# Kernel optimization log

Measured on AMD Instinct MI355X. Metric: run time of the kernel, lower is better.

Reference implementation:

```python
import jax, jax.numpy as jnp
import numpy as np

N = 50000
E = 800000
IN_DIM = 256
HID = 128
HALF = HID // 2
OUT_DIM = 2


def setup_inputs() -> dict:
    key = jax.random.key(0)
    ks = jax.random.split(key, 16)
    s = lambda fan_in: 1.0 / np.sqrt(fan_in)
    inp = {
        "x": jax.random.normal(ks[0], (N, IN_DIM), dtype=jnp.float32),
        "edge_index": jax.random.randint(ks[1], (2, E), 0, N, dtype=jnp.int64),
        # lin_in: input_dim -> hidden
        "W_in": jax.random.uniform(ks[2], (IN_DIM, HID), jnp.float32, -s(IN_DIM), s(IN_DIM)),
        "b_in": jnp.zeros((HID,), jnp.float32),
        # lin_nor / lin_abnor: half -> hidden
        "W_nor": jax.random.uniform(ks[3], (HALF, HID), jnp.float32, -s(HALF), s(HALF)),
        "b_nor": jnp.zeros((HID,), jnp.float32),
        "W_abnor": jax.random.uniform(ks[4], (HALF, HID), jnp.float32, -s(HALF), s(HALF)),
        "b_abnor": jnp.zeros((HID,), jnp.float32),
        # attention gate
        "W_att": jax.random.uniform(ks[5], (HID, HID), jnp.float32, -s(HID), s(HID)),
        "b_att": jnp.zeros((HID,), jnp.float32),
        "v_att": jax.random.uniform(ks[6], (HID, 1), jnp.float32, -s(HID), s(HID)),
        # update linear
        "W_upd": jax.random.uniform(ks[7], (HID, HID), jnp.float32, -s(HID), s(HID)),
        "b_upd": jnp.zeros((HID,), jnp.float32),
        # classifier
        "W_cls": jax.random.uniform(ks[8], (HID, OUT_DIM), jnp.float32, -s(HID), s(HID)),
        "b_cls": jnp.zeros((OUT_DIM,), jnp.float32),
    }
    return inp


def reference(x, edge_index, W_in, b_in, W_nor, b_nor, W_abnor, b_abnor,
              W_att, b_att, v_att, W_upd, b_upd, W_cls, b_cls):
    n = x.shape[0]
    # add self loops (add_self_loops)
    loops = jnp.tile(jnp.arange(n, dtype=edge_index.dtype), (2, 1))
    ei = jnp.concatenate([edge_index, loops], axis=1)
    row, col = ei[0], ei[1]  # row = source j, col = target i

    # lin_in + leaky_relu (dropout p=0 / eval)
    h = jax.nn.leaky_relu(x @ W_in + b_in)

    # split halves and project
    x_nor = h[:, :HALF] @ W_nor + b_nor      # [N, HID]
    x_abnor = h[:, HALF:] @ W_abnor + b_abnor

    # symmetric normalization by target degree
    deg = jax.ops.segment_sum(jnp.ones_like(col, dtype=h.dtype), col, num_segments=n)
    dinv = jnp.where(deg > 0, jax.lax.rsqrt(jnp.where(deg > 0, deg, 1.0)), 0.0)
    norm = dinv[row] * dinv[col]             # [E']

    # per-edge gather
    xn_j = x_nor[row]                        # [E', HID]
    xa_j = x_abnor[row]

    # denoising attention gate: sigmoid(v^T tanh(W(xn+xa)+b))
    h_att = jnp.tanh((xn_j + xa_j) @ W_att + b_att)
    alpha = jax.nn.sigmoid(h_att @ v_att)    # [E', 1]

    msg = norm[:, None] * (alpha * xn_j + (1.0 - alpha) * xa_j)

    # scatter-add to targets
    aggr = jax.ops.segment_sum(msg, col, num_segments=n)  # [N, HID]

    upd = aggr @ W_upd + b_upd
    out = jax.nn.leaky_relu(upd) @ W_cls + b_cls
    return out
```

## Files before the change

kernel.cpp:

```cpp
#include <hip/hip_runtime.h>

#define N_NODES 50000
#define E_EDGES 800000
#define IN_DIM  256
#define HID     128
#define HALF    64
#define OUT_DIM 2
#define NW      32
#define SLOPE   0.01f

#define ST      132
#define WSLICE  (NW * ST)

#define SSTRIDE 520
#define PLANE   (8 * SSTRIDE)

#define SCAN_B  512
#define SCAN_NB ((N_NODES + SCAN_B - 1) / SCAN_B)

typedef unsigned int uint32;
typedef __attribute__((ext_vector_type(8)))  __bf16 bf16x8v;
typedef __attribute__((ext_vector_type(16))) float  f32x16;

union BF8 { bf16x8v v; unsigned short s[8]; uint4 q; };

#define FI_F 0
#define FN_F 4096
#define FA_F 5120
#define FT_F 6144
#define FU_F 8192
#define F_TOTAL 10240

__device__ __forceinline__ uint32 rne16u(uint32 u) {
    return (u + 0x7fffu + ((u >> 16) & 1u)) >> 16;
}

__device__ __forceinline__ uint32 pack_hl(float v) {
    uint32 uu = __float_as_uint(v);
    uint32 hh = rne16u(uu);
    float  fh = __uint_as_float(hh << 16);
    float  r  = v - fh;
    uint32 ll = rne16u(__float_as_uint(r));
    return (hh << 16) | ll;
}

__device__ __forceinline__ float fast_tanh(float x) {
    float ex = __expf(2.f * x);
    return 1.f - 2.f * __builtin_amdgcn_rcpf(ex + 1.f);
}
__device__ __forceinline__ float fast_sig(float x) {
    return __builtin_amdgcn_rcpf(1.f + __expf(-x));
}

__device__ __forceinline__ void mfma3(f32x16& acc, bf16x8v ah, bf16x8v al,
                                      bf16x8v bh, bf16x8v bl) {
    acc = __builtin_amdgcn_mfma_f32_32x32x16_bf16(ah, bh, acc, 0, 0, 0);
    acc = __builtin_amdgcn_mfma_f32_32x32x16_bf16(ah, bl, acc, 0, 0, 0);
    acc = __builtin_amdgcn_mfma_f32_32x32x16_bf16(al, bh, acc, 0, 0, 0);
}

__device__ __forceinline__ void stage_split4(__bf16* __restrict__ Ahi,
                                             __bf16* __restrict__ Alo,
                                             int rr, int k, float4 v) {
    int s_idx = k >> 4, jb = k & 7, lt = rr + 32 * ((k >> 3) & 1);
    int base = s_idx * SSTRIDE + lt * 8 + jb;
    float f[4] = {v.x, v.y, v.z, v.w};
    uint32 h[4], lo[4];
    #pragma unroll
    for (int j = 0; j < 4; j++) {
        uint32 uu = __float_as_uint(f[j]);
        uint32 hh = rne16u(uu);
        float  fh = __uint_as_float(hh << 16);
        float  r  = f[j] - fh;
        h[j] = hh; lo[j] = rne16u(__float_as_uint(r));
    }
    *(uint2*)(Ahi + base) = make_uint2(h[0] | (h[1] << 16), h[2] | (h[3] << 16));
    *(uint2*)(Alo + base) = make_uint2(lo[0] | (lo[1] << 16), lo[2] | (lo[3] << 16));
}

__device__ __forceinline__ void mfma_gemm1_pre(f32x16& acc,
        const __bf16* __restrict__ Ahi, const __bf16* __restrict__ Alo,
        int S, int sg0, const uint4* __restrict__ F, int fbase, int l, int t) {
    for (int s = 0; s < S; s++) {
        bf16x8v ah = *(const bf16x8v*)&Ahi[s * SSTRIDE + l * 8];
        bf16x8v al = *(const bf16x8v*)&Alo[s * SSTRIDE + l * 8];
        int f = fbase + ((sg0 + s) * 4 + t) * 64 + l;
        BF8 bh, bl; bh.q = F[2 * f]; bl.q = F[2 * f + 1];
        mfma3(acc, ah, al, bh.v, bl.v);
    }
}

__device__ __forceinline__ void mfma_gemm1_pk(f32x16& acc, const uint32* T,
        int aoff, int S, const uint4* __restrict__ F, int fbase, int l, int t) {
    const int row = l & 31, khi = 8 * (l >> 5);
    for (int s = 0; s < S; s++) {
        int k0 = aoff + 16 * s + khi;
        uint4 qa = *(const uint4*)&T[row * ST + k0];
        uint4 qb = *(const uint4*)&T[row * ST + k0 + 4];
        BF8 ah, al;
        ah.q.x = (qa.x >> 16) | (qa.y & 0xffff0000u);
        ah.q.y = (qa.z >> 16) | (qa.w & 0xffff0000u);
        ah.q.z = (qb.x >> 16) | (qb.y & 0xffff0000u);
        ah.q.w = (qb.z >> 16) | (qb.w & 0xffff0000u);
        al.q.x = (qa.x & 0xffffu) | (qa.y << 16);
        al.q.y = (qa.z & 0xffffu) | (qa.w << 16);
        al.q.z = (qb.x & 0xffffu) | (qb.y << 16);
        al.q.w = (qb.z & 0xffffu) | (qb.w << 16);
        int f = fbase + (s * 4 + t) * 64 + l;
        BF8 bh, bl; bh.q = F[2 * f]; bl.q = F[2 * f + 1];
        mfma3(acc, ah.v, al.v, bh.v, bl.v);
    }
}

__device__ __forceinline__ uint32 pack_bf2(float x, float y) {
    return rne16u(__float_as_uint(x)) | (rne16u(__float_as_uint(y)) << 16);
}

__global__ void zero_int_kernel(int* __restrict__ p, int n) {
    int i = blockIdx.x * blockDim.x + threadIdx.x;
    if (i < n) p[i] = 0;
}

__global__ void deg_ticket_kernel(const int* __restrict__ col,
                                  int* __restrict__ cnt, int* __restrict__ ticket) {
    int e = blockIdx.x * blockDim.x + threadIdx.x;
    if (e < E_EDGES) ticket[e] = atomicAdd(&cnt[col[e]], 1);
}

__device__ __forceinline__ int wave_iscan(int v, int l) {
    #pragma unroll
    for (int off = 1; off < 64; off <<= 1) {
        int t = __shfl_up(v, off, 64);
        if (l >= off) v += t;
    }
    return v;
}

__global__ __launch_bounds__(SCAN_B) void scan1_kernel(
    const int* __restrict__ cnt, int* __restrict__ row_start, int* __restrict__ bsum)
{
    __shared__ int wsum[SCAN_B / 64];
    int i = blockIdx.x * SCAN_B + threadIdx.x;
    int v = (i < N_NODES) ? cnt[i] : 0;
    int l = threadIdx.x & 63, w = threadIdx.x >> 6;
    int isc = wave_iscan(v, l);
    if (l == 63) wsum[w] = isc;
    __syncthreads();
    int wo = 0;
    #pragma unroll
    for (int k = 0; k < SCAN_B / 64; k++) wo += (k < w) ? wsum[k] : 0;
    if (i < N_NODES) row_start[i] = wo + isc - v;
    if (threadIdx.x == SCAN_B - 1) bsum[blockIdx.x] = wo + isc;
}

__global__ __launch_bounds__(128) void scan2_kernel(
    int* __restrict__ bsum, int* __restrict__ row_start)
{
    __shared__ int wsum[2];
    int i = threadIdx.x;
    int v = (i < SCAN_NB) ? bsum[i] : 0;
    int l = i & 63, w = i >> 6;
    int isc = wave_iscan(v, l);
    if (l == 63) wsum[w] = isc;
    __syncthreads();
    int wo = (w == 1) ? wsum[0] : 0;
    if (i < SCAN_NB) bsum[i] = wo + isc - v;
    if (i == SCAN_NB - 1) row_start[N_NODES] = wo + isc;
}

__global__ __launch_bounds__(SCAN_B) void scan3_kernel(
    const int* __restrict__ bsum, int* __restrict__ row_start)
{
    int i = blockIdx.x * SCAN_B + threadIdx.x;
    if (i < N_NODES) row_start[i] += bsum[blockIdx.x];
}

__global__ void fill_kernel(const int* __restrict__ ei,
                            const int* __restrict__ row_start,
                            const int* __restrict__ ticket,
                            int* __restrict__ csr_src)
{
    int e = blockIdx.x * blockDim.x + threadIdx.x;
    if (e >= E_EDGES) return;
    int j = ei[e];
    int i = ei[E_EDGES + e];
    csr_src[row_start[i] + ticket[e]] = j;
}

__global__ __launch_bounds__(256) void prep_w_kernel(
    const float* __restrict__ W_in, const float* __restrict__ W_nor,
    const float* __restrict__ W_ab, const float* __restrict__ W_att,
    const float* __restrict__ W_upd,
    uint4* __restrict__ F)
{
    int idx = blockIdx.x * 256 + threadIdx.x;
    const float* W; int fbase, fi;
    if (idx < 4096)       { W = W_in;  fbase = FI_F; fi = idx; }
    else if (idx < 5120)  { W = W_nor; fbase = FN_F; fi = idx - 4096; }
    else if (idx < 6144)  { W = W_ab;  fbase = FA_F; fi = idx - 5120; }
    else if (idx < 8192)  { W = W_att; fbase = FT_F; fi = idx - 6144; }
    else if (idx < 10240) { W = W_upd; fbase = FU_F; fi = idx - 8192; }
    else return;
    int l = fi & 63, st = fi >> 6, t = st & 3, s = st >> 2;
    int k0 = 16 * s + 8 * (l >> 5);
    int c  = 32 * t + (l & 31);
    uint32 hi[8], lo[8];
    #pragma unroll
    for (int j = 0; j < 8; j++) {
        float v = W[(size_t)(k0 + j) * HID + c];
        uint32 uu = __float_as_uint(v);
        uint32 h  = rne16u(uu);
        float  fh = __uint_as_float(h << 16);
        float  r  = v - fh;
        hi[j] = h;
        lo[j] = rne16u(__float_as_uint(r));
    }
    uint4 H, L;
    H.x = hi[0] | (hi[1] << 16); H.y = hi[2] | (hi[3] << 16);
    H.z = hi[4] | (hi[5] << 16); H.w = hi[6] | (hi[7] << 16);
    L.x = lo[0] | (lo[1] << 16); L.y = lo[2] | (lo[3] << 16);
    L.z = lo[4] | (lo[5] << 16); L.w = lo[6] | (lo[7] << 16);
    int f = fbase + fi;
    F[2 * f]     = H;
    F[2 * f + 1] = L;
}

__global__ __launch_bounds__(256, 4) void node_phase_kernel(
    const float* __restrict__ x,
    const float* __restrict__ b_in,  const float* __restrict__ b_nor,
    const float* __restrict__ b_abnor, const float* __restrict__ b_att,
    const float* __restrict__ v_att,
    const int* __restrict__ cnt,
    const uint4* __restrict__ F,
    uint32* __restrict__ u)
{
    __shared__ __align__(16) float smem[WSLICE];
    __shared__ float dinvs[NW];
    __shared__ float gpart[4][NW];
    __bf16* Ahi = (__bf16*)smem;
    __bf16* Alo = (__bf16*)smem + PLANE;
    uint32* T   = (uint32*)smem;

    const int tid    = threadIdx.x;
    const int w      = tid >> 6;
    const int l      = tid & 63;
    const int col    = l & 31;
    const int hi     = l >> 5;
    const int wnode0 = blockIdx.x * NW;

    if (tid < NW) {
        int nd = wnode0 + tid;
        float c = (nd < N_NODES) ? (float)cnt[nd] : 0.f;
        dinvs[tid] = rsqrtf(c + 1.0f);
    }

    f32x16 hacc;
    {
        float bv = b_in[32 * w + col];
        #pragma unroll
        for (int r2 = 0; r2 < 16; r2++) hacc[r2] = bv;
    }
    for (int half = 0; half < 2; half++) {
        #pragma unroll
        for (int it = 0; it < 4; it++) {
            int i = it * 256 + tid;
            int rr = i >> 5, kq = i & 31, k = 4 * kq;
            int nd = wnode0 + rr; if (nd >= N_NODES) nd = N_NODES - 1;
            float4 v = *(const float4*)(x + (size_t)nd * IN_DIM + half * 128 + k);
            stage_split4(Ahi, Alo, rr, k, v);
        }
        __syncthreads();
        mfma_gemm1_pre(hacc, Ahi, Alo, 8, half * 8, F, FI_F, l, w);
        __syncthreads();
    }

    #pragma unroll
    for (int rg = 0; rg < 16; rg++) {
        int rrow = (rg & 3) + 8 * (rg >> 2) + 4 * hi;
        float v = hacc[rg];
        v = v > 0.f ? v : SLOPE * v;
        T[rrow * ST + 32 * w + col] = pack_hl(v);
    }
    __syncthreads();

    f32x16 xn, xa;
    {
        float bv = b_nor[32 * w + col];
        #pragma unroll
        for (int r2 = 0; r2 < 16; r2++) xn[r2] = bv;
    }
    mfma_gemm1_pk(xn, T, 0, 4, F, FN_F, l, w);
    {
        float bv = b_abnor[32 * w + col];
        #pragma unroll
        for (int r2 = 0; r2 < 16; r2++) xa[r2] = bv;
    }
    mfma_gemm1_pk(xa, T, HALF, 4, F, FA_F, l, w);
    __syncthreads();

    f32x16 sv, d;
    #pragma unroll
    for (int rg = 0; rg < 16; rg++) {
        int rrow = (rg & 3) + 8 * (rg >> 2) + 4 * hi;
        sv[rg] = xn[rg] + xa[rg];
        d[rg]  = xn[rg] - xa[rg];
        T[rrow * ST + 32 * w + col] = pack_hl(sv[rg]);
    }
    __syncthreads();

    f32x16 tac;
    {
        float bv = b_att[32 * w + col];
        #pragma unroll
        for (int r2 = 0; r2 < 16; r2++) tac[r2] = bv;
    }
    mfma_gemm1_pk(tac, T, 0, 8, F, FT_F, l, w);

    float g[16];
    {
        float vv = v_att[32 * w + col];
        #pragma unroll
        for (int rg = 0; rg < 16; rg++) g[rg] = fast_tanh(tac[rg]) * vv;
    }
    #pragma unroll
    for (int msk = 16; msk >= 1; msk >>= 1) {
        #pragma unroll
        for (int rg = 0; rg < 16; rg++) g[rg] += __shfl_xor(g[rg], msk, 64);
    }
    if (col == 0) {
        #pragma unroll
        for (int rg = 0; rg < 16; rg++) {
            int rrow = (rg & 3) + 8 * (rg >> 2) + 4 * hi;
            gpart[w][rrow] = g[rg];
        }
    }
    __syncthreads();

    float am[16];
    #pragma unroll
    for (int rg = 0; rg < 16; rg++) {
        int rrow = (rg & 3) + 8 * (rg >> 2) + 4 * hi;
        float gt = gpart[0][rrow] + gpart[1][rrow] + gpart[2][rrow] + gpart[3][rrow];
        am[rg] = fast_sig(gt) - 0.5f;
    }

    #pragma unroll
    for (int rg = 0; rg < 16; rg++) {
        int rrow = (rg & 3) + 8 * (rg >> 2) + 4 * hi;
        int n    = wnode0 + rrow;
        float uv = dinvs[rrow] * (0.5f * sv[rg] + am[rg] * d[rg]);
        float pv = __shfl_xor(uv, 1, 64);
        if (((l & 1) == 0) && n < N_NODES) {
            u[(size_t)n * (HID / 2) + 16 * w + (col >> 1)] = pack_bf2(uv, pv);
        }
    }
}

__global__ __launch_bounds__(256, 4) void final_fused_kernel(
    const int* __restrict__ row_start, const int* __restrict__ csr_src,
    const uint32* __restrict__ u, const int* __restrict__ cnt,
    const float* __restrict__ b_upd,
    const float* __restrict__ W_cls, const float* __restrict__ b_cls,
    const uint4* __restrict__ F,
    float* __restrict__ out)
{
    __shared__ __align__(16) float smem[WSLICE];
    __bf16* Ahi = (__bf16*)smem;
    __bf16* Alo = (__bf16*)smem + PLANE;

    const int tid    = threadIdx.x;
    const int w      = tid >> 6;
    const int l      = tid & 63;
    const int col    = l & 31;
    const int hi     = l >> 5;
    const int wnode0 = blockIdx.x * NW;

    const size_t RW = HID / 2;
    const int kk   = 2 * l;
    const int sidx = kk >> 4, jj = kk & 7, ltb = 32 * ((kk >> 3) & 1);

    for (int q = 0; q < 8; q++) {
        int rr = 8 * w + q;
        int nd = wnode0 + rr; if (nd >= N_NODES) nd = N_NODES - 1;

        uint32 v = u[(size_t)nd * RW + l];
        float sx = __uint_as_float(v << 16);
        float sy = __uint_as_float(v & 0xffff0000u);

        int b = row_start[nd], e = row_start[nd + 1];
        for (int p = b; p < e; p += 8) {
            int idx[8];
            #pragma unroll
            for (int qq = 0; qq < 8; qq++) {
                int a = p + qq; if (a > e - 1) a = e - 1;
                idx[qq] = csr_src[a];
            }
            uint32 vv[8];
            #pragma unroll
            for (int qq = 0; qq < 8; qq++) vv[qq] = u[(size_t)idx[qq] * RW + l];
            #pragma unroll
            for (int qq = 0; qq < 8; qq++) {
                if (p + qq < e) {
                    sx += __uint_as_float(vv[qq] << 16);
                    sy += __uint_as_float(vv[qq] & 0xffff0000u);
                }
            }
        }
        float dv = rsqrtf((float)cnt[nd] + 1.0f);
        sx *= dv; sy *= dv;

        uint32 px = pack_hl(sx), py = pack_hl(sy);
        int base = sidx * SSTRIDE + (rr + ltb) * 8 + jj;
        *(uint32*)&Ahi[base] = (px >> 16) | (py & 0xffff0000u);
        *(uint32*)&Alo[base] = (px & 0xffffu) | (py << 16);
    }
    __syncthreads();

    f32x16 up;
    {
        float bv = b_upd[32 * w + col];
        #pragma unroll
        for (int r2 = 0; r2 < 16; r2++) up[r2] = bv;
    }
    mfma_gemm1_pre(up, Ahi, Alo, 8, 0, F, FU_F, l, w);
    __syncthreads();

    float* B = smem;
    #pragma unroll
    for (int rg = 0; rg < 16; rg++) {
        int rrow = (rg & 3) + 8 * (rg >> 2) + 4 * hi;
        float v = up[rg];
        B[rrow * ST + 32 * w + col] = v > 0.f ? v : SLOPE * v;
    }
    __syncthreads();

    {
        int n = tid >> 3, o = (tid >> 2) & 1, c = tid & 3;
        float s = 0.f;
        int k0 = c * 32;
        for (int k = k0; k < k0 + 32; k++)
            s = fmaf(B[n * ST + k], W_cls[k * OUT_DIM + o], s);
        s += __shfl_xor(s, 1, 64);
        s += __shfl_xor(s, 2, 64);
        if (c == 0 && wnode0 + n < N_NODES) {
            out[(size_t)(wnode0 + n) * OUT_DIM + o] = s + b_cls[o];
        }
    }
}

extern "C" void kernel_launch(void* const* d_in, const int* in_sizes, int n_in,
                              void* d_out, int out_size, void* d_ws, size_t ws_size,
                              hipStream_t stream)
{
    const float* x       = (const float*)d_in[0];
    const int*   ei      = (const int*)  d_in[1];
    const float* W_in    = (const float*)d_in[2];
    const float* b_in    = (const float*)d_in[3];
    const float* W_nor   = (const float*)d_in[4];
    const float* b_nor   = (const float*)d_in[5];
    const float* W_abnor = (const float*)d_in[6];
    const float* b_abnor = (const float*)d_in[7];
    const float* W_att   = (const float*)d_in[8];
    const float* b_att   = (const float*)d_in[9];
    const float* v_att   = (const float*)d_in[10];
    const float* W_upd   = (const float*)d_in[11];
    const float* b_upd   = (const float*)d_in[12];
    const float* W_cls   = (const float*)d_in[13];
    const float* b_cls   = (const float*)d_in[14];
    float* out = (float*)d_out;

    char* base = (char*)d_ws;
    int*  cnt       = (int*)base;
    int*  row_start = cnt + N_NODES;
    int*  bsum      = row_start + (N_NODES + 1);
    int*  csr_src   = bsum + 128;
    int*  ticket    = csr_src + E_EDGES;
    size_t off_u    = (((size_t)(2 * N_NODES + 129 + 2 * E_EDGES)) * 4 + 63) & ~(size_t)63;
    uint32* u       = (uint32*)(base + off_u);
    size_t off_f    = (off_u + (size_t)N_NODES * (HID / 2) * 4 + 63) & ~(size_t)63;
    uint4* F        = (uint4*)(base + off_f);

    const int nblk = (N_NODES + NW - 1) / NW;

    zero_int_kernel<<<(N_NODES + 255) / 256, 256, 0, stream>>>(cnt, N_NODES);
    deg_ticket_kernel<<<(E_EDGES + 255) / 256, 256, 0, stream>>>(ei + E_EDGES, cnt, ticket);
    scan1_kernel<<<SCAN_NB, SCAN_B, 0, stream>>>(cnt, row_start, bsum);
    scan2_kernel<<<1, 128, 0, stream>>>(bsum, row_start);
    scan3_kernel<<<SCAN_NB, SCAN_B, 0, stream>>>(bsum, row_start);
    fill_kernel<<<(E_EDGES + 255) / 256, 256, 0, stream>>>(ei, row_start, ticket, csr_src);
    prep_w_kernel<<<F_TOTAL / 256, 256, 0, stream>>>(W_in, W_nor, W_abnor, W_att, W_upd, F);
    node_phase_kernel<<<nblk, 256, 0, stream>>>(
        x, b_in, b_nor, b_abnor, b_att, v_att, cnt, F, u);
    final_fused_kernel<<<nblk, 256, 0, stream>>>(
        row_start, csr_src, u, cnt, b_upd, W_cls, b_cls, F, out);
}
```

Before: 159.9 us.

## Interleave neighbor gathers across eight nodes per wave to raise memory parallelism

The per-wave aggregation loop previously handled its eight target nodes one after another, issuing up to eight gathers per node. It now keeps eight accumulators and walks all eight nodes' neighbor lists together in steps of four, so each iteration issues 32 independent gathers. The aim is more memory-level parallelism and less exposed latency in the irregular gather. The cost is higher register pressure, and wasted clamped loads for nodes whose lists are shorter than the longest one in the group.

```diff
diff --git a/kernel.cpp b/kernel.cpp
--- a/kernel.cpp
+++ b/kernel.cpp
@@ -379,37 +379,56 @@
     const int kk   = 2 * l;
     const int sidx = kk >> 4, jj = kk & 7, ltb = 32 * ((kk >> 3) & 1);
 
+    int nd_[8], bq[8], eq[8];
+    float sx[8], sy[8];
+    #pragma unroll
     for (int q = 0; q < 8; q++) {
         int rr = 8 * w + q;
         int nd = wnode0 + rr; if (nd >= N_NODES) nd = N_NODES - 1;
-
+        nd_[q] = nd;
+        bq[q] = row_start[nd];
+        eq[q] = row_start[nd + 1];
         uint32 v = u[(size_t)nd * RW + l];
-        float sx = __uint_as_float(v << 16);
-        float sy = __uint_as_float(v & 0xffff0000u);
-
-        int b = row_start[nd], e = row_start[nd + 1];
-        for (int p = b; p < e; p += 8) {
-            int idx[8];
+        sx[q] = __uint_as_float(v << 16);
+        sy[q] = __uint_as_float(v & 0xffff0000u);
+    }
+    int mb = 0;
+    #pragma unroll
+    for (int q = 0; q < 8; q++) {
+        int nb = (eq[q] - bq[q] + 3) >> 2;
+        mb = nb > mb ? nb : mb;
+    }
+
+    for (int bt = 0; bt < mb; bt++) {
+        uint32 vv[8][4];
+        #pragma unroll
+        for (int q = 0; q < 8; q++) {
             #pragma unroll
-            for (int qq = 0; qq < 8; qq++) {
-                int a = p + qq; if (a > e - 1) a = e - 1;
-                idx[qq] = csr_src[a];
+            for (int j = 0; j < 4; j++) {
+                int p = bq[q] + 4 * bt + j;
+                int a = p > eq[q] - 1 ? eq[q] - 1 : p;
+                int idx = csr_src[a];
+                vv[q][j] = u[(size_t)idx * RW + l];
             }
-            uint32 vv[8];
+        }
+        #pragma unroll
+        for (int q = 0; q < 8; q++) {
             #pragma unroll
-            for (int qq = 0; qq < 8; qq++) vv[qq] = u[(size_t)idx[qq] * RW + l];
-            #pragma unroll
-            for (int qq = 0; qq < 8; qq++) {
-                if (p + qq < e) {
-                    sx += __uint_as_float(vv[qq] << 16);
-                    sy += __uint_as_float(vv[qq] & 0xffff0000u);
+            for (int j = 0; j < 4; j++) {
+                if (bq[q] + 4 * bt + j < eq[q]) {
+                    sx[q] += __uint_as_float(vv[q][j] << 16);
+                    sy[q] += __uint_as_float(vv[q][j] & 0xffff0000u);
                 }
             }
         }
-        float dv = rsqrtf((float)cnt[nd] + 1.0f);
-        sx *= dv; sy *= dv;
-
-        uint32 px = pack_hl(sx), py = pack_hl(sy);
+    }
+
+    #pragma unroll
+    for (int q = 0; q < 8; q++) {
+        int rr = 8 * w + q;
+        float dv = rsqrtf((float)cnt[nd_[q]] + 1.0f);
+        float fx = sx[q] * dv, fy = sy[q] * dv;
+        uint32 px = pack_hl(fx), py = pack_hl(fy);
         int base = sidx * SSTRIDE + (rr + ltb) * 8 + jj;
         *(uint32*)&Ahi[base] = (px >> 16) | (py & 0xffff0000u);
         *(uint32*)&Alo[base] = (px & 0xffffu) | (py << 16);
```

Result: slower. 167.1 us (+4.5%).
